# Kernel optimization log

Measured on AMD Instinct MI355X. Metric: run time of the kernel, lower is better.

## Reference

```python
import jax, jax.numpy as jnp
import numpy as np

B, S, D, H, F = 8, 1024, 1024, 16, 4096
DH = D // H  # 64
EPS = 1e-5


def layer_norm(x, g, b):
    mu = jnp.mean(x, axis=-1, keepdims=True)
    var = jnp.mean(jnp.square(x - mu), axis=-1, keepdims=True)
    return (x - mu) * jax.lax.rsqrt(var + EPS) * g + b


def mha(q_in, k_in, v_in, wq, wk, wv, wo, causal):
    # wq/wk/wv: [H, D, DH] (stacked per-head nn.Linear weights, pre-transposed)
    Q = jnp.einsum('bsd,hdk->bhsk', q_in, wq)
    K = jnp.einsum('bsd,hdk->bhsk', k_in, wk)
    V = jnp.einsum('bsd,hdk->bhsk', v_in, wv)
    scores = jnp.einsum('bhsk,bhtk->bhst', Q, K) / jnp.sqrt(jnp.asarray(DH, Q.dtype))
    if causal:
        mask = jnp.triu(jnp.ones((S, S), dtype=bool), k=1)  # True = inaccessible
        scores = jnp.where(mask, -jnp.inf, scores)
    A = jax.nn.softmax(scores, axis=-1)
    heads = jnp.einsum('bhst,bhtk->bhsk', A, V)
    heads = heads.transpose(0, 2, 1, 3).reshape(q_in.shape[0], q_in.shape[1], D)
    return heads @ wo.T  # nn.Linear convention


def setup_inputs() -> dict:
    key = jax.random.key(0)
    ks = jax.random.split(key, 16)
    sc = 1.0 / np.sqrt(D)
    scf = 1.0 / np.sqrt(F)
    return {
        'embeds': jax.random.normal(ks[0], (B, S, D), jnp.float32),
        'encoder_output': jax.random.normal(ks[1], (B, S, D), jnp.float32),
        'wq1': jax.random.normal(ks[2], (H, D, DH), jnp.float32) * sc,
        'wk1': jax.random.normal(ks[3], (H, D, DH), jnp.float32) * sc,
        'wv1': jax.random.normal(ks[4], (H, D, DH), jnp.float32) * sc,
        'wo1': jax.random.normal(ks[5], (D, D), jnp.float32) * sc,
        'wq2': jax.random.normal(ks[6], (H, D, DH), jnp.float32) * sc,
        'wk2': jax.random.normal(ks[7], (H, D, DH), jnp.float32) * sc,
        'wv2': jax.random.normal(ks[8], (H, D, DH), jnp.float32) * sc,
        'wo2': jax.random.normal(ks[9], (D, D), jnp.float32) * sc,
        'ln1_g': jnp.ones((D,), jnp.float32), 'ln1_b': jnp.zeros((D,), jnp.float32),
        'ln2_g': jnp.ones((D,), jnp.float32), 'ln2_b': jnp.zeros((D,), jnp.float32),
        'ln3_g': jnp.ones((D,), jnp.float32), 'ln3_b': jnp.zeros((D,), jnp.float32),
        'w1': jax.random.normal(ks[10], (F, D), jnp.float32) * sc,
        'b1': jnp.zeros((F,), jnp.float32),
        'w2': jax.random.normal(ks[11], (D, F), jnp.float32) * scf,
        'b2': jnp.zeros((D,), jnp.float32),
    }


def reference(embeds, encoder_output, wq1, wk1, wv1, wo1, wq2, wk2, wv2, wo2,
              ln1_g, ln1_b, ln2_g, ln2_b, ln3_g, ln3_b, w1, b1, w2, b2):
    # masked (causal) self-attention + residual + LN
    sa = mha(embeds, embeds, embeds, wq1, wk1, wv1, wo1, causal=True)
    x1 = layer_norm(sa + embeds, ln1_g, ln1_b)
    # cross-attention (no mask) + residual + LN
    ca = mha(x1, encoder_output, encoder_output, wq2, wk2, wv2, wo2, causal=False)
    x2 = layer_norm(ca + x1, ln2_g, ln2_b)
    # feedforward (Linear -> GELU(exact) -> Linear) + residual + LN
    ff = jax.nn.gelu(x2 @ w1.T + b1, approximate=False) @ w2.T + b2
    return layer_norm(ff + x2, ln3_g, ln3_b)
```

## Files before the change

kernel.cpp:

```cpp
#include <hip/hip_runtime.h>
#include <cstdint>
#include <cstddef>

typedef unsigned short u16;
typedef __attribute__((ext_vector_type(4))) float f32x4;
typedef __attribute__((ext_vector_type(4))) float f4;
typedef __attribute__((ext_vector_type(8))) short short8x;
typedef __attribute__((ext_vector_type(4))) u16 u16x4;
typedef __attribute__((ext_vector_type(8))) u16 u16x8;

#define DEV static __device__ __forceinline__

DEV void gl_lds16(const void* g, void* l) {
  __builtin_amdgcn_global_load_lds(
      (const __attribute__((address_space(1))) unsigned int*)g,
      (__attribute__((address_space(3))) unsigned int*)l, 16, 0, 0);
}

DEV u16 f2bf(float f) {
  unsigned u = __float_as_uint(f);
  u += 0x7fffu + ((u >> 16) & 1u);
  return (u16)(u >> 16);
}


__global__ __launch_bounds__(256) void cast_bf16(const float* __restrict__ X, u16* __restrict__ Y) {
  size_t i = ((size_t)blockIdx.x * 256 + threadIdx.x) * 4;
  f4 v = *(const f4*)(X + i);
  u16x4 y;
#pragma unroll
  for (int j = 0; j < 4; ++j) y[j] = f2bf(v[j]);
  *(u16x4*)(Y + i) = y;
}

__global__ __launch_bounds__(256) void cast_wqkv(const float* __restrict__ W, u16* __restrict__ Wt) {
  __shared__ float tile[64][65];
  const int t = threadIdx.x;
  const int h = blockIdx.y;
  const int d0 = blockIdx.x * 64;
  const float* Wb = W + (size_t)h * (1024 * 64);
  const int di = t >> 2;
  const int j0 = (t & 3) * 16;
#pragma unroll
  for (int c = 0; c < 4; ++c) {
    f4 v = *(const f4*)(Wb + (size_t)(d0 + di) * 64 + j0 + c * 4);
#pragma unroll
    for (int j = 0; j < 4; ++j) tile[di][j0 + c * 4 + j] = v[j];
  }
  __syncthreads();
  const int k = t >> 2;
  const int dd0 = (t & 3) * 16;
  u16x8 o0, o1;
#pragma unroll
  for (int u = 0; u < 8; ++u) o0[u] = f2bf(tile[dd0 + u][k]);
#pragma unroll
  for (int u = 0; u < 8; ++u) o1[u] = f2bf(tile[dd0 + 8 + u][k]);
  u16* dst = Wt + (size_t)(h * 64 + k) * 1024 + d0 + dd0;
  *(u16x8*)(dst) = o0;
  *(u16x8*)(dst + 8) = o1;
}

__global__ __launch_bounds__(256) void transpose_v(const u16* __restrict__ V, u16* __restrict__ Vt,
                                                   int vstride, int voff) {
  __shared__ u16 tile[32][72];
  const int t = threadIdx.x;
  const int bh = blockIdx.y;
  const int s0 = blockIdx.x * 32;
  const u16* Vb = V + (size_t)(bh >> 4) * (1024 * (size_t)vstride) + voff + (bh & 15) * 64;
  const int si = t >> 3, d0 = (t & 7) * 8;
  u16x8 val = *(const u16x8*)(Vb + (size_t)(s0 + si) * vstride + d0);
#pragma unroll
  for (int u = 0; u < 8; ++u) tile[si][d0 + u] = val[u];
  __syncthreads();
  const int d = t >> 2, sj0 = (t & 3) * 8;
  u16x8 o;
#pragma unroll
  for (int u = 0; u < 8; ++u) o[u] = tile[sj0 + u][d];
  *(u16x8*)(Vt + (size_t)bh * (64 * 1024) + (size_t)d * 1024 + s0 + sj0) = o;
}

template <int EPI>
__global__ __launch_bounds__(256, 3) void gemm_bt(const u16* __restrict__ A, const u16* __restrict__ Bt,
                                                  void* __restrict__ C, const float* __restrict__ bias,
                                                  int M, int N, int K, int ldc) {
  __shared__ u16 As[2][128 * 32];
  __shared__ u16 Bs[2][128 * 32];
  const int t = threadIdx.x;
  const int wave = t >> 6, lane = t & 63;
  const int lr = lane & 15, lkg = lane >> 4;
  const int swz = (lr >> 1) & 3;
  const int wr = (wave >> 1) * 64, wc = (wave & 1) * 64;
  const int m0 = blockIdx.y * 128, n0 = blockIdx.x * 128;

  const int schunk = ((t & 3) ^ ((t >> 3) & 3)) << 4;
  const char* gA = (const char*)(A + (size_t)(m0 + (t >> 2)) * K) + schunk;
  const char* gB = (const char*)(Bt + (size_t)(n0 + (t >> 2)) * K) + schunk;
  const size_t rowskip = (size_t)64 * K * 2;

  const f32x4 fzero = {0.f, 0.f, 0.f, 0.f};
  f32x4 acc[4][4];
#pragma unroll
  for (int m = 0; m < 4; ++m)
#pragma unroll
    for (int n = 0; n < 4; ++n) acc[m][n] = fzero;

  const int nk = K >> 5;

  auto stage = [&](int buf, int kt) {
    const size_t kb = (size_t)kt * 64;
    char* la = ((char*)&As[buf][0]) + wave * 1024;
    char* lb = ((char*)&Bs[buf][0]) + wave * 1024;
    gl_lds16(gA + kb, la);
    gl_lds16(gA + kb + rowskip, la + 4096);
    gl_lds16(gB + kb, lb);
    gl_lds16(gB + kb + rowskip, lb + 4096);
  };

  auto compute = [&](int buf) {
    const char* as = (const char*)&As[buf][0];
    const char* bs = (const char*)&Bs[buf][0];
    short8x aF[4], bF[4];
#pragma unroll
    for (int m = 0; m < 4; ++m)
      aF[m] = *(const short8x*)(as + (size_t)(wr + m * 16 + lr) * 64 + ((lkg ^ swz) << 4));
#pragma unroll
    for (int n = 0; n < 4; ++n)
      bF[n] = *(const short8x*)(bs + (size_t)(wc + n * 16 + lr) * 64 + ((lkg ^ swz) << 4));
#pragma unroll
    for (int m = 0; m < 4; ++m)
#pragma unroll
      for (int n = 0; n < 4; ++n)
        acc[m][n] = __builtin_amdgcn_mfma_f32_16x16x32_bf16(aF[m], bF[n], acc[m][n], 0, 0, 0);
  };

  stage(0, 0);
  __syncthreads();
  int cur = 0;
  for (int kt = 0; kt < nk; ++kt) {
    if (kt + 1 < nk) stage(cur ^ 1, kt + 1);
    compute(cur);
    __syncthreads();
    cur ^= 1;
  }

#pragma unroll
  for (int m = 0; m < 4; ++m) {
#pragma unroll
    for (int rr = 0; rr < 4; ++rr) {
      const int gm = m0 + wr + m * 16 + lkg * 4 + rr;
#pragma unroll
      for (int n = 0; n < 4; ++n) {
        const int gn = n0 + wc + n * 16 + lr;
        float v = acc[m][n][rr];
        if (EPI == 2 || EPI == 3) v += bias[gn];
        if (EPI == 2) v = 0.5f * v * (1.0f + erff(v * 0.70710678118654752f));
        if (EPI == 4) v *= 0.125f;
        if (EPI == 5 && gn < 1024) v *= 0.125f;
        if (EPI == 1 || EPI == 3)
          ((float*)C)[(size_t)gm * ldc + gn] = v;
        else
          ((u16*)C)[(size_t)gm * ldc + gn] = f2bf(v);
      }
    }
  }
}

template <int CAUSAL>
__global__ __launch_bounds__(256, 2) void flash_attn(const u16* __restrict__ Q, const u16* __restrict__ Kk,
                                                     const u16* __restrict__ Vt, u16* __restrict__ O,
                                                     int qst) {
  __shared__ u16 Ks[2][64 * 64];
  __shared__ u16 Vs[2][64 * 64];
  __shared__ u16 Ps[4][32 * 72];
  const int t = threadIdx.x;
  const int wave = t >> 6, lane = t & 63;
  const int lr = lane & 15, lkg = lane >> 4, lk = lkg * 8;
  const int sw = lr & 7;
  const int bh = blockIdx.y;
  const size_t base = (size_t)(bh >> 4) * (1024 * (size_t)qst) + (bh & 15) * 64;
  const u16* Qb = Q + base;
  const u16* Kb = Kk + base;
  const u16* Vtb = Vt + (size_t)bh * (64 * 1024);
  u16* Ob = O + (size_t)(bh >> 4) * (1024 * 1024) + (bh & 15) * 64;
  const int qt = blockIdx.x * 128;
  const int qw = qt + wave * 32;

  const f32x4 fzero = {0.f, 0.f, 0.f, 0.f};
  short8x qf[2][2];
#pragma unroll
  for (int rb = 0; rb < 2; ++rb)
#pragma unroll
    for (int kk = 0; kk < 2; ++kk)
      qf[rb][kk] = *(const short8x*)(Qb + (size_t)(qw + rb * 16 + lr) * qst + kk * 32 + lk);

  float m_[2][4], l_[2][4];
  f32x4 o_[2][4];
#pragma unroll
  for (int rb = 0; rb < 2; ++rb) {
#pragma unroll
    for (int rr = 0; rr < 4; ++rr) { m_[rb][rr] = -1e30f; l_[rb][rr] = 0.f; }
#pragma unroll
    for (int db = 0; db < 4; ++db) o_[rb][db] = fzero;
  }

  const int rsel = lane >> 3;
  const int csw = ((lane & 7) ^ rsel) << 4;

  auto stage = [&](int buf, int kv0) {
#pragma unroll
    for (int s = 0; s < 2; ++s) {
      const int row = s * 32 + wave * 8 + rsel;
      gl_lds16((const char*)Kb + (size_t)(kv0 + row) * (size_t)(qst * 2) + csw,
               (char*)&Ks[buf][0] + s * 4096 + wave * 1024);
      gl_lds16((const char*)Vtb + (size_t)row * 2048 + (size_t)kv0 * 2 + csw,
               (char*)&Vs[buf][0] + s * 4096 + wave * 1024);
    }
  };

  const int kv_end = CAUSAL ? (qt + 128) : 1024;
  const int nt = kv_end >> 6;

  stage(0, 0);
  __syncthreads();
  int cur = 0;
  for (int tt = 0; tt < nt; ++tt) {
    const int kv0 = tt * 64;
    if (tt + 1 < nt) stage(cur ^ 1, kv0 + 64);

    const char* ksb = (const char*)&Ks[cur][0];
    const char* vsb = (const char*)&Vs[cur][0];

    short8x kf[4][2];
#pragma unroll
    for (int nb = 0; nb < 4; ++nb) {
      const int row = nb * 16 + lr;
#pragma unroll
      for (int kk = 0; kk < 2; ++kk)
        kf[nb][kk] = *(const short8x*)(ksb + row * 128 + (((kk * 4 + lkg) ^ sw) << 4));
    }

#pragma unroll
    for (int rb = 0; rb < 2; ++rb) {
      f32x4 s[4];
#pragma unroll
      for (int nb = 0; nb < 4; ++nb) {
        s[nb] = __builtin_amdgcn_mfma_f32_16x16x32_bf16(qf[rb][0], kf[nb][0], fzero, 0, 0, 0);
        s[nb] = __builtin_amdgcn_mfma_f32_16x16x32_bf16(qf[rb][1], kf[nb][1], s[nb], 0, 0, 0);
      }
      if (CAUSAL && (kv0 + 63 > qw + rb * 16)) {
#pragma unroll
        for (int rr = 0; rr < 4; ++rr) {
          const int qg = qw + rb * 16 + lkg * 4 + rr;
#pragma unroll
          for (int nb = 0; nb < 4; ++nb)
            if (kv0 + nb * 16 + lr > qg) s[nb][rr] = -1e30f;
        }
      }
#pragma unroll
      for (int rr = 0; rr < 4; ++rr) {
        float mx = fmaxf(fmaxf(s[0][rr], s[1][rr]), fmaxf(s[2][rr], s[3][rr]));
#pragma unroll
        for (int d = 1; d < 16; d <<= 1) mx = fmaxf(mx, __shfl_xor(mx, d, 16));
        const float mold = m_[rb][rr];
        const float mnew = fmaxf(mold, mx);
        float p[4];
#pragma unroll
        for (int nb = 0; nb < 4; ++nb) p[nb] = __expf(s[nb][rr] - mnew);
        float rsum = (p[0] + p[1]) + (p[2] + p[3]);
#pragma unroll
        for (int d = 1; d < 16; d <<= 1) rsum += __shfl_xor(rsum, d, 16);
        const float alpha = __expf(mold - mnew);
        m_[rb][rr] = mnew;
        l_[rb][rr] = l_[rb][rr] * alpha + rsum;
#pragma unroll
        for (int db = 0; db < 4; ++db) o_[rb][db][rr] *= alpha;
        const int prow = rb * 16 + lkg * 4 + rr;
#pragma unroll
        for (int nb = 0; nb < 4; ++nb)
          Ps[wave][prow * 72 + nb * 16 + lr] = f2bf(p[nb]);
      }
    }
    asm volatile("s_waitcnt lgkmcnt(0)" ::: "memory");

    short8x vF[4][2];
#pragma unroll
    for (int db = 0; db < 4; ++db) {
      const int row = db * 16 + lr;
#pragma unroll
      for (int kk = 0; kk < 2; ++kk)
        vF[db][kk] = *(const short8x*)(vsb + row * 128 + (((kk * 4 + lkg) ^ sw) << 4));
    }
#pragma unroll
    for (int rb = 0; rb < 2; ++rb) {
#pragma unroll
      for (int kk = 0; kk < 2; ++kk) {
        const short8x aP = *(const short8x*)((const char*)&Ps[wave][0] + (rb * 16 + lr) * 144 + kk * 64 + lkg * 16);
#pragma unroll
        for (int db = 0; db < 4; ++db)
          o_[rb][db] = __builtin_amdgcn_mfma_f32_16x16x32_bf16(aP, vF[db][kk], o_[rb][db], 0, 0, 0);
      }
    }
    __syncthreads();
    cur ^= 1;
  }

#pragma unroll
  for (int rb = 0; rb < 2; ++rb)
#pragma unroll
    for (int rr = 0; rr < 4; ++rr) {
      const float inv = 1.0f / l_[rb][rr];
      const int qg = qw + rb * 16 + lkg * 4 + rr;
#pragma unroll
      for (int db = 0; db < 4; ++db)
        Ob[(size_t)qg * 1024 + db * 16 + lr] = f2bf(o_[rb][db][rr] * inv);
    }
}

__global__ __launch_bounds__(256) void ln_res(const float* __restrict__ X, const float* __restrict__ R,
                                              const float* __restrict__ gam, const float* __restrict__ bet,
                                              float* __restrict__ oF, u16* __restrict__ oB) {
  __shared__ float red[8];
  const int row = blockIdx.x, t = threadIdx.x;
  const int wave = t >> 6, lane = t & 63;
  const size_t off = (size_t)row * 1024 + t * 4;
  f4 x = *(const f4*)(X + off);
  f4 r = *(const f4*)(R + off);
  float v[4];
  float s = 0.f, sq = 0.f;
#pragma unroll
  for (int j = 0; j < 4; ++j) {
    v[j] = x[j] + r[j];
    s += v[j];
    sq += v[j] * v[j];
  }
#pragma unroll
  for (int d = 1; d < 64; d <<= 1) {
    s += __shfl_xor(s, d, 64);
    sq += __shfl_xor(sq, d, 64);
  }
  if (lane == 0) { red[wave * 2] = s; red[wave * 2 + 1] = sq; }
  __syncthreads();
  s = red[0] + red[2] + red[4] + red[6];
  sq = red[1] + red[3] + red[5] + red[7];
  const float mu = s * (1.0f / 1024.0f);
  const float var = sq * (1.0f / 1024.0f) - mu * mu;
  const float rs = rsqrtf(var + 1e-5f);
  f4 g4 = *(const f4*)(gam + t * 4);
  f4 b4 = *(const f4*)(bet + t * 4);
  f4 y;
#pragma unroll
  for (int j = 0; j < 4; ++j) y[j] = (v[j] - mu) * rs * g4[j] + b4[j];
  *(f4*)(oF + off) = y;
  if (oB) {
    u16x4 yb;
#pragma unroll
    for (int j = 0; j < 4; ++j) yb[j] = f2bf(y[j]);
    *(u16x4*)(oB + off) = yb;
  }
}

extern "C" void kernel_launch(void* const* d_in, const int* in_sizes, int n_in,
                              void* d_out, int out_size, void* d_ws, size_t ws_size,
                              hipStream_t stream) {
  const float* embeds = (const float*)d_in[0];
  const float* enc = (const float*)d_in[1];
  const float* wq1 = (const float*)d_in[2];
  const float* wk1 = (const float*)d_in[3];
  const float* wv1 = (const float*)d_in[4];
  const float* wo1 = (const float*)d_in[5];
  const float* wq2 = (const float*)d_in[6];
  const float* wk2 = (const float*)d_in[7];
  const float* wv2 = (const float*)d_in[8];
  const float* wo2 = (const float*)d_in[9];
  const float* ln1g = (const float*)d_in[10];
  const float* ln1b = (const float*)d_in[11];
  const float* ln2g = (const float*)d_in[12];
  const float* ln2b = (const float*)d_in[13];
  const float* ln3g = (const float*)d_in[14];
  const float* ln3b = (const float*)d_in[15];
  const float* w1 = (const float*)d_in[16];
  const float* b1 = (const float*)d_in[17];
  const float* w2 = (const float*)d_in[18];
  const float* b2 = (const float*)d_in[19];
  float* out = (float*)d_out;
  char* ws = (char*)d_ws;
  const size_t MB = (size_t)1 << 20;

  u16* QKV = (u16*)(ws + 0 * MB);
  u16* Vtb = (u16*)(ws + 48 * MB);
  u16* Hd = (u16*)(ws + 64 * MB);
  float* Of = (float*)(ws + 80 * MB);
  u16* ebf = (u16*)(ws + 112 * MB);
  u16* encb = (u16*)(ws + 128 * MB);
  float* x1f = (float*)(ws + 144 * MB);
  float* x2f = (float*)(ws + 176 * MB);
  u16* Wq1t = (u16*)(ws + 208 * MB);
  u16* Wk1t = (u16*)(ws + 210 * MB);
  u16* Wv1t = (u16*)(ws + 212 * MB);
  u16* Wo1b = (u16*)(ws + 214 * MB);
  u16* Wq2t = (u16*)(ws + 216 * MB);
  u16* Wk2t = (u16*)(ws + 218 * MB);
  u16* Wv2t = (u16*)(ws + 220 * MB);
  u16* Wo2b = (u16*)(ws + 222 * MB);
  u16* W1b = (u16*)(ws + 224 * MB);
  u16* W2b = (u16*)(ws + 232 * MB);
  u16* x1b = ebf;
  u16* x2b = encb;
  u16* Hff = (u16*)(ws + 0 * MB);

  dim3 blk(256);

  cast_bf16<<<8192, blk, 0, stream>>>(embeds, ebf);
  cast_bf16<<<8192, blk, 0, stream>>>(enc, encb);
  cast_wqkv<<<dim3(16, 16), blk, 0, stream>>>(wq1, Wq1t);
  cast_wqkv<<<dim3(16, 16), blk, 0, stream>>>(wk1, Wk1t);
  cast_wqkv<<<dim3(16, 16), blk, 0, stream>>>(wv1, Wv1t);
  cast_wqkv<<<dim3(16, 16), blk, 0, stream>>>(wq2, Wq2t);
  cast_wqkv<<<dim3(16, 16), blk, 0, stream>>>(wk2, Wk2t);
  cast_wqkv<<<dim3(16, 16), blk, 0, stream>>>(wv2, Wv2t);
  cast_bf16<<<1024, blk, 0, stream>>>(wo1, Wo1b);
  cast_bf16<<<1024, blk, 0, stream>>>(wo2, Wo2b);
  cast_bf16<<<4096, blk, 0, stream>>>(w1, W1b);
  cast_bf16<<<4096, blk, 0, stream>>>(w2, W2b);

  gemm_bt<5><<<dim3(24, 64), blk, 0, stream>>>(ebf, Wq1t, QKV, nullptr, 8192, 3072, 1024, 3072);
  transpose_v<<<dim3(32, 128), blk, 0, stream>>>(QKV, Vtb, 3072, 2048);
  flash_attn<1><<<dim3(8, 128), blk, 0, stream>>>(QKV, QKV + 1024, Vtb, Hd, 3072);
  gemm_bt<1><<<dim3(8, 64), blk, 0, stream>>>(Hd, Wo1b, Of, nullptr, 8192, 1024, 1024, 1024);
  ln_res<<<8192, blk, 0, stream>>>(Of, embeds, ln1g, ln1b, x1f, x1b);

  gemm_bt<4><<<dim3(8, 64), blk, 0, stream>>>(x1b, Wq2t, QKV, nullptr, 8192, 1024, 1024, 3072);
  gemm_bt<0><<<dim3(16, 64), blk, 0, stream>>>(encb, Wk2t, QKV + 1024, nullptr, 8192, 2048, 1024, 3072);
  transpose_v<<<dim3(32, 128), blk, 0, stream>>>(QKV, Vtb, 3072, 2048);
  flash_attn<0><<<dim3(8, 128), blk, 0, stream>>>(QKV, QKV + 1024, Vtb, Hd, 3072);
  gemm_bt<1><<<dim3(8, 64), blk, 0, stream>>>(Hd, Wo2b, Of, nullptr, 8192, 1024, 1024, 1024);
  ln_res<<<8192, blk, 0, stream>>>(Of, x1f, ln2g, ln2b, x2f, x2b);

  gemm_bt<2><<<dim3(32, 64), blk, 0, stream>>>(x2b, W1b, Hff, b1, 8192, 4096, 1024, 4096);
  gemm_bt<3><<<dim3(8, 64), blk, 0, stream>>>(Hff, W2b, Of, b2, 8192, 1024, 4096, 1024);
  ln_res<<<8192, blk, 0, stream>>>(Of, x2f, ln3g, ln3b, out, nullptr);
}
```

Measured before the change: 762.8 us.

## Replace 128x128 GEMM with 256x256 eight-wave pipelined GEMM

Swaps the 128x128-tile, 4-wave GEMM for a 256x256-tile, 8-wave kernel with K-step 64. It issues split global-to-LDS loads interleaved with MFMA phases, using explicit vmcnt and lgkmcnt waits, barriers and setprio. Workgroup IDs are remapped so consecutive blocks spread across XCDs. The aim is more data reuse per tile and better overlap of loads with matrix math, at the cost of fewer workgroups (e.g. 128 for N=1024 GEMMs), which may leave CUs underused on a 256-CU part.

```diff
diff --git a/kernel.cpp b/kernel.cpp
--- a/kernel.cpp
+++ b/kernel.cpp
@@ -10,6 +10,8 @@
 typedef __attribute__((ext_vector_type(8))) u16 u16x8;
 
 #define DEV static __device__ __forceinline__
+#define VMC(n) asm volatile("s_waitcnt vmcnt(" #n ")" ::: "memory")
+#define LG0() asm volatile("s_waitcnt lgkmcnt(0)" ::: "memory")
 
 DEV void gl_lds16(const void* g, void* l) {
   __builtin_amdgcn_global_load_lds(
@@ -80,77 +82,128 @@
 }
 
 template <int EPI>
-__global__ __launch_bounds__(256, 3) void gemm_bt(const u16* __restrict__ A, const u16* __restrict__ Bt,
+__global__ __launch_bounds__(512, 2) void gemm256(const u16* __restrict__ A, const u16* __restrict__ Bt,
                                                   void* __restrict__ C, const float* __restrict__ bias,
                                                   int M, int N, int K, int ldc) {
-  __shared__ u16 As[2][128 * 32];
-  __shared__ u16 Bs[2][128 * 32];
+  __shared__ u16 lds[65536];
+  char* ldsA = (char*)lds;
+  char* ldsB = (char*)lds + 65536;
   const int t = threadIdx.x;
   const int wave = t >> 6, lane = t & 63;
+  const int wr = wave >> 2, wc = wave & 3;
   const int lr = lane & 15, lkg = lane >> 4;
-  const int swz = (lr >> 1) & 3;
-  const int wr = (wave >> 1) * 64, wc = (wave & 1) * 64;
-  const int m0 = blockIdx.y * 128, n0 = blockIdx.x * 128;
-
-  const int schunk = ((t & 3) ^ ((t >> 3) & 3)) << 4;
-  const char* gA = (const char*)(A + (size_t)(m0 + (t >> 2)) * K) + schunk;
-  const char* gB = (const char*)(Bt + (size_t)(n0 + (t >> 2)) * K) + schunk;
-  const size_t rowskip = (size_t)64 * K * 2;
+  const int swz = lr & 7;
+
+  const int gx = gridDim.x;
+  const int nwg = gx * gridDim.y;
+  const int flat = blockIdx.y * gx + blockIdx.x;
+  const int wg = ((nwg & 7) == 0) ? ((flat & 7) * (nwg >> 3) + (flat >> 3)) : flat;
+  const int m0 = (wg / gx) * 256;
+  const int n0 = (wg % gx) * 256;
+
+  const int nk = K >> 6;
+  const size_t rowb = (size_t)K * 2;
+
+  const int srow = wave * 8 + (lane >> 3);
+  const int sgc = ((lane & 7) ^ (srow & 7)) << 4;
+  const char* gA = (const char*)A + (size_t)(m0 + srow) * rowb + sgc;
+  const char* gB = (const char*)Bt + (size_t)(n0 + srow) * rowb + sgc;
+
+  auto stgA = [&](int kt, int q) {
+    if (kt < nk)
+      gl_lds16(gA + (size_t)(q * 64) * rowb + (size_t)kt * 128,
+               ldsA + ((kt & 1) << 15) + (q << 13) + (wave << 10));
+  };
+  auto stgB = [&](int kt, int q) {
+    if (kt < nk)
+      gl_lds16(gB + (size_t)(q * 64) * rowb + (size_t)kt * 128,
+               ldsB + ((kt & 1) << 15) + (q << 13) + (wave << 10));
+  };
 
   const f32x4 fzero = {0.f, 0.f, 0.f, 0.f};
-  f32x4 acc[4][4];
-#pragma unroll
-  for (int m = 0; m < 4; ++m)
+  f32x4 acc[8][4];
+#pragma unroll
+  for (int m = 0; m < 8; ++m)
 #pragma unroll
     for (int n = 0; n < 4; ++n) acc[m][n] = fzero;
 
-  const int nk = K >> 5;
-
-  auto stage = [&](int buf, int kt) {
-    const size_t kb = (size_t)kt * 64;
-    char* la = ((char*)&As[buf][0]) + wave * 1024;
-    char* lb = ((char*)&Bs[buf][0]) + wave * 1024;
-    gl_lds16(gA + kb, la);
-    gl_lds16(gA + kb + rowskip, la + 4096);
-    gl_lds16(gB + kb, lb);
-    gl_lds16(gB + kb + rowskip, lb + 4096);
-  };
-
-  auto compute = [&](int buf) {
-    const char* as = (const char*)&As[buf][0];
-    const char* bs = (const char*)&Bs[buf][0];
-    short8x aF[4], bF[4];
-#pragma unroll
-    for (int m = 0; m < 4; ++m)
-      aF[m] = *(const short8x*)(as + (size_t)(wr + m * 16 + lr) * 64 + ((lkg ^ swz) << 4));
-#pragma unroll
-    for (int n = 0; n < 4; ++n)
-      bF[n] = *(const short8x*)(bs + (size_t)(wc + n * 16 + lr) * 64 + ((lkg ^ swz) << 4));
-#pragma unroll
-    for (int m = 0; m < 4; ++m)
-#pragma unroll
-      for (int n = 0; n < 4; ++n)
-        acc[m][n] = __builtin_amdgcn_mfma_f32_16x16x32_bf16(aF[m], bF[n], acc[m][n], 0, 0, 0);
-  };
-
-  stage(0, 0);
-  __syncthreads();
-  int cur = 0;
+  stgA(0, 0); stgA(0, 2);
+  stgB(0, 0); stgB(0, 1); stgB(0, 2); stgB(0, 3);
+  stgA(0, 1); stgA(0, 3);
+  stgA(1, 0); stgA(1, 2);
+  VMC(4);
+  __builtin_amdgcn_s_barrier();
+
   for (int kt = 0; kt < nk; ++kt) {
-    if (kt + 1 < nk) stage(cur ^ 1, kt + 1);
-    compute(cur);
-    __syncthreads();
-    cur ^= 1;
-  }
-
-#pragma unroll
-  for (int m = 0; m < 4; ++m) {
+    const char* aB = ldsA + ((kt & 1) << 15);
+    const char* bB = ldsB + ((kt & 1) << 15);
+    short8x aF[4][2], bF[2][2];
+
+    auto rdA = [&](int mh) {
+#pragma unroll
+      for (int mq = 0; mq < 4; ++mq)
+#pragma unroll
+        for (int kh = 0; kh < 2; ++kh)
+          aF[mq][kh] = *(const short8x*)(aB + ((wr * 2 + mh) << 13) + (mq * 16 + lr) * 128 +
+                                         (((kh * 4 + lkg) ^ swz) << 4));
+    };
+    auto rdB = [&](int nh) {
+#pragma unroll
+      for (int nq = 0; nq < 2; ++nq)
+#pragma unroll
+        for (int kh = 0; kh < 2; ++kh)
+          bF[nq][kh] = *(const short8x*)(bB + (wc << 13) + (nh * 32 + nq * 16 + lr) * 128 +
+                                         (((kh * 4 + lkg) ^ swz) << 4));
+    };
+    auto mma = [&](int mh, int nh) {
+      __builtin_amdgcn_s_setprio(1);
+#pragma unroll
+      for (int kh = 0; kh < 2; ++kh)
+#pragma unroll
+        for (int mq = 0; mq < 4; ++mq)
+#pragma unroll
+          for (int nq = 0; nq < 2; ++nq)
+            acc[mh * 4 + mq][nh * 2 + nq] = __builtin_amdgcn_mfma_f32_16x16x32_bf16(
+                aF[mq][kh], bF[nq][kh], acc[mh * 4 + mq][nh * 2 + nq], 0, 0, 0);
+      __builtin_amdgcn_s_setprio(0);
+    };
+
+    rdA(0); rdB(0);
+    stgB(kt + 1, 0); stgB(kt + 1, 1);
+    __builtin_amdgcn_s_barrier();
+    LG0();
+    mma(0, 0);
+    __builtin_amdgcn_s_barrier();
+    rdB(1);
+    stgB(kt + 1, 2); stgB(kt + 1, 3);
+    __builtin_amdgcn_s_barrier();
+    LG0();
+    mma(0, 1);
+    if (kt + 1 < nk) { VMC(6); } else { VMC(0); }
+    __builtin_amdgcn_s_barrier();
+    rdA(1); rdB(0);
+    stgA(kt + 1, 1); stgA(kt + 1, 3);
+    stgA(kt + 2, 0); stgA(kt + 2, 2);
+    __builtin_amdgcn_s_barrier();
+    LG0();
+    mma(1, 0);
+    __builtin_amdgcn_s_barrier();
+    rdB(1);
+    __builtin_amdgcn_s_barrier();
+    LG0();
+    mma(1, 1);
+    if (kt + 2 < nk) { VMC(4); } else if (kt + 1 < nk) { VMC(2); } else { VMC(0); }
+    __builtin_amdgcn_s_barrier();
+  }
+
+#pragma unroll
+  for (int m = 0; m < 8; ++m) {
 #pragma unroll
     for (int rr = 0; rr < 4; ++rr) {
-      const int gm = m0 + wr + m * 16 + lkg * 4 + rr;
+      const int gm = m0 + wr * 128 + m * 16 + lkg * 4 + rr;
 #pragma unroll
       for (int n = 0; n < 4; ++n) {
-        const int gn = n0 + wc + n * 16 + lr;
+        const int gn = n0 + wc * 64 + n * 16 + lr;
         float v = acc[m][n][rr];
         if (EPI == 2 || EPI == 3) v += bias[gn];
         if (EPI == 2) v = 0.5f * v * (1.0f + erff(v * 0.70710678118654752f));
@@ -409,6 +462,7 @@
   u16* Hff = (u16*)(ws + 0 * MB);
 
   dim3 blk(256);
+  dim3 blk512(512);
 
   cast_bf16<<<8192, blk, 0, stream>>>(embeds, ebf);
   cast_bf16<<<8192, blk, 0, stream>>>(enc, encb);
@@ -423,20 +477,20 @@
   cast_bf16<<<4096, blk, 0, stream>>>(w1, W1b);
   cast_bf16<<<4096, blk, 0, stream>>>(w2, W2b);
 
-  gemm_bt<5><<<dim3(24, 64), blk, 0, stream>>>(ebf, Wq1t, QKV, nullptr, 8192, 3072, 1024, 3072);
+  gemm256<5><<<dim3(12, 32), blk512, 0, stream>>>(ebf, Wq1t, QKV, nullptr, 8192, 3072, 1024, 3072);
   transpose_v<<<dim3(32, 128), blk, 0, stream>>>(QKV, Vtb, 3072, 2048);
   flash_attn<1><<<dim3(8, 128), blk, 0, stream>>>(QKV, QKV + 1024, Vtb, Hd, 3072);
-  gemm_bt<1><<<dim3(8, 64), blk, 0, stream>>>(Hd, Wo1b, Of, nullptr, 8192, 1024, 1024, 1024);
+  gemm256<1><<<dim3(4, 32), blk512, 0, stream>>>(Hd, Wo1b, Of, nullptr, 8192, 1024, 1024, 1024);
   ln_res<<<8192, blk, 0, stream>>>(Of, embeds, ln1g, ln1b, x1f, x1b);
 
-  gemm_bt<4><<<dim3(8, 64), blk, 0, stream>>>(x1b, Wq2t, QKV, nullptr, 8192, 1024, 1024, 3072);
-  gemm_bt<0><<<dim3(16, 64), blk, 0, stream>>>(encb, Wk2t, QKV + 1024, nullptr, 8192, 2048, 1024, 3072);
+  gemm256<4><<<dim3(4, 32), blk512, 0, stream>>>(x1b, Wq2t, QKV, nullptr, 8192, 1024, 1024, 3072);
+  gemm256<0><<<dim3(8, 32), blk512, 0, stream>>>(encb, Wk2t, QKV + 1024, nullptr, 8192, 2048, 1024, 3072);
   transpose_v<<<dim3(32, 128), blk, 0, stream>>>(QKV, Vtb, 3072, 2048);
   flash_attn<0><<<dim3(8, 128), blk, 0, stream>>>(QKV, QKV + 1024, Vtb, Hd, 3072);
-  gemm_bt<1><<<dim3(8, 64), blk, 0, stream>>>(Hd, Wo2b, Of, nullptr, 8192, 1024, 1024, 1024);
+  gemm256<1><<<dim3(4, 32), blk512, 0, stream>>>(Hd, Wo2b, Of, nullptr, 8192, 1024, 1024, 1024);
   ln_res<<<8192, blk, 0, stream>>>(Of, x1f, ln2g, ln2b, x2f, x2b);
 
-  gemm_bt<2><<<dim3(32, 64), blk, 0, stream>>>(x2b, W1b, Hff, b1, 8192, 4096, 1024, 4096);
-  gemm_bt<3><<<dim3(8, 64), blk, 0, stream>>>(Hff, W2b, Of, b2, 8192, 1024, 4096, 1024);
+  gemm256<2><<<dim3(16, 32), blk512, 0, stream>>>(x2b, W1b, Hff, b1, 8192, 4096, 1024, 4096);
+  gemm256<3><<<dim3(4, 32), blk512, 0, stream>>>(Hff, W2b, Of, b2, 8192, 1024, 4096, 1024);
   ln_res<<<8192, blk, 0, stream>>>(Of, x2f, ln3g, ln3b, out, nullptr);
 }
```

Measured after the change: 943.5 us. 23.7% more time.

## Replace GEMM with larger 256-row tile, 512-thread kernel with XCD-aware block remap

Applied to the files above, without the earlier changes.

Replaces the 128x128, 256-thread GEMM with a 512-thread kernel using 256xBN tiles and a K-step of 64. It uses an 8-way XOR LDS swizzle, explicit waitcnt, sched_barrier and setprio around the MFMA bursts, and a workgroup index remap that groups blocks by XCD. The aim is more data reuse per LDS load, fewer barriers per K, and better L2 locality on the multi-die GPU. The cost is larger LDS and register use per block (up to 128 KB LDS for BN=256), which lowers occupancy and leaves fewer blocks in the grid for tail balancing.

```diff
diff --git a/kernel.cpp b/kernel.cpp
--- a/kernel.cpp
+++ b/kernel.cpp
@@ -10,6 +10,8 @@
 typedef __attribute__((ext_vector_type(8))) u16 u16x8;
 
 #define DEV static __device__ __forceinline__
+#define VMC0() asm volatile("s_waitcnt vmcnt(0)" ::: "memory")
+#define LG0() asm volatile("s_waitcnt lgkmcnt(0)" ::: "memory")
 
 DEV void gl_lds16(const void* g, void* l) {
   __builtin_amdgcn_global_load_lds(
@@ -79,78 +81,101 @@
   *(u16x8*)(Vt + (size_t)bh * (64 * 1024) + (size_t)d * 1024 + s0 + sj0) = o;
 }
 
-template <int EPI>
-__global__ __launch_bounds__(256, 3) void gemm_bt(const u16* __restrict__ A, const u16* __restrict__ Bt,
+template <int EPI, int BN>
+__global__ __launch_bounds__(512, 2) void gemm2ph(const u16* __restrict__ A, const u16* __restrict__ Bt,
                                                   void* __restrict__ C, const float* __restrict__ bias,
-                                                  int M, int N, int K, int ldc) {
-  __shared__ u16 As[2][128 * 32];
-  __shared__ u16 Bs[2][128 * 32];
+                                                  int K, int ldc) {
+  constexpr int NBQ = BN / 64;
+  constexpr int MR = (BN == 256) ? 8 : 4;
+  __shared__ char ldsA[2][32768];
+  __shared__ char ldsB[2][BN * 128];
+
   const int t = threadIdx.x;
   const int wave = t >> 6, lane = t & 63;
+  const int wr = (BN == 256) ? (wave >> 2) : (wave >> 1);
+  const int wc = (BN == 256) ? (wave & 3) : (wave & 1);
   const int lr = lane & 15, lkg = lane >> 4;
-  const int swz = (lr >> 1) & 3;
-  const int wr = (wave >> 1) * 64, wc = (wave & 1) * 64;
-  const int m0 = blockIdx.y * 128, n0 = blockIdx.x * 128;
-
-  const int schunk = ((t & 3) ^ ((t >> 3) & 3)) << 4;
-  const char* gA = (const char*)(A + (size_t)(m0 + (t >> 2)) * K) + schunk;
-  const char* gB = (const char*)(Bt + (size_t)(n0 + (t >> 2)) * K) + schunk;
-  const size_t rowskip = (size_t)64 * K * 2;
+  const int swz = lr & 7;
+
+  const int gx = gridDim.x;
+  const int nwg = gx * gridDim.y;
+  const int flat = blockIdx.y * gx + blockIdx.x;
+  const int wg = ((nwg & 7) == 0) ? ((flat & 7) * (nwg >> 3) + (flat >> 3)) : flat;
+  const int m0 = (wg / gx) * 256;
+  const int n0 = (wg % gx) * BN;
+
+  const int nk = K >> 6;
+  const size_t rowb = (size_t)K * 2;
+
+  const int srow = wave * 8 + (lane >> 3);
+  const int sgc = ((lane & 7) ^ (srow & 7)) << 4;
+  const char* gA = (const char*)A + (size_t)(m0 + srow) * rowb + sgc;
+  const char* gB = (const char*)Bt + (size_t)(n0 + srow) * rowb + sgc;
+
+  auto stageTile = [&](int buf, int kt) {
+    const size_t kb = (size_t)kt * 128;
+    char* la = &ldsA[buf][0] + (wave << 10);
+    char* lb = &ldsB[buf][0] + (wave << 10);
+#pragma unroll
+    for (int q = 0; q < 4; ++q)
+      gl_lds16(gA + (size_t)(q * 64) * rowb + kb, la + q * 8192);
+#pragma unroll
+    for (int q = 0; q < NBQ; ++q)
+      gl_lds16(gB + (size_t)(q * 64) * rowb + kb, lb + q * 8192);
+  };
 
   const f32x4 fzero = {0.f, 0.f, 0.f, 0.f};
-  f32x4 acc[4][4];
-#pragma unroll
-  for (int m = 0; m < 4; ++m)
+  f32x4 acc[MR][4];
+#pragma unroll
+  for (int m = 0; m < MR; ++m)
 #pragma unroll
     for (int n = 0; n < 4; ++n) acc[m][n] = fzero;
 
-  const int nk = K >> 5;
-
-  auto stage = [&](int buf, int kt) {
-    const size_t kb = (size_t)kt * 64;
-    char* la = ((char*)&As[buf][0]) + wave * 1024;
-    char* lb = ((char*)&Bs[buf][0]) + wave * 1024;
-    gl_lds16(gA + kb, la);
-    gl_lds16(gA + kb + rowskip, la + 4096);
-    gl_lds16(gB + kb, lb);
-    gl_lds16(gB + kb + rowskip, lb + 4096);
-  };
-
-  auto compute = [&](int buf) {
-    const char* as = (const char*)&As[buf][0];
-    const char* bs = (const char*)&Bs[buf][0];
-    short8x aF[4], bF[4];
-#pragma unroll
-    for (int m = 0; m < 4; ++m)
-      aF[m] = *(const short8x*)(as + (size_t)(wr + m * 16 + lr) * 64 + ((lkg ^ swz) << 4));
-#pragma unroll
-    for (int n = 0; n < 4; ++n)
-      bF[n] = *(const short8x*)(bs + (size_t)(wc + n * 16 + lr) * 64 + ((lkg ^ swz) << 4));
-#pragma unroll
-    for (int m = 0; m < 4; ++m)
-#pragma unroll
-      for (int n = 0; n < 4; ++n)
-        acc[m][n] = __builtin_amdgcn_mfma_f32_16x16x32_bf16(aF[m], bF[n], acc[m][n], 0, 0, 0);
-  };
-
-  stage(0, 0);
-  __syncthreads();
+  stageTile(0, 0);
+  VMC0();
+  __builtin_amdgcn_s_barrier();
+
   int cur = 0;
   for (int kt = 0; kt < nk; ++kt) {
-    if (kt + 1 < nk) stage(cur ^ 1, kt + 1);
-    compute(cur);
-    __syncthreads();
+    if (kt + 1 < nk) stageTile(cur ^ 1, kt + 1);
+    const char* aB = &ldsA[cur][0];
+    const char* bB = &ldsB[cur][0];
+#pragma unroll
+    for (int kh = 0; kh < 2; ++kh) {
+      short8x aF[MR], bF[4];
+#pragma unroll
+      for (int m = 0; m < MR; ++m) {
+        const int row = wr * (MR * 16) + m * 16 + lr;
+        aF[m] = *(const short8x*)(aB + row * 128 + (((kh * 4 + lkg) ^ swz) << 4));
+      }
+#pragma unroll
+      for (int n = 0; n < 4; ++n) {
+        const int row = wc * 64 + n * 16 + lr;
+        bF[n] = *(const short8x*)(bB + row * 128 + (((kh * 4 + lkg) ^ swz) << 4));
+      }
+      LG0();
+      __builtin_amdgcn_sched_barrier(0);
+      __builtin_amdgcn_s_setprio(1);
+#pragma unroll
+      for (int m = 0; m < MR; ++m)
+#pragma unroll
+        for (int n = 0; n < 4; ++n)
+          acc[m][n] = __builtin_amdgcn_mfma_f32_16x16x32_bf16(aF[m], bF[n], acc[m][n], 0, 0, 0);
+      __builtin_amdgcn_s_setprio(0);
+    }
+    VMC0();
+    __builtin_amdgcn_s_barrier();
     cur ^= 1;
   }
 
 #pragma unroll
-  for (int m = 0; m < 4; ++m) {
+  for (int m = 0; m < MR; ++m) {
 #pragma unroll
     for (int rr = 0; rr < 4; ++rr) {
-      const int gm = m0 + wr + m * 16 + lkg * 4 + rr;
+      const int gm = m0 + wr * (MR * 16) + m * 16 + lkg * 4 + rr;
 #pragma unroll
       for (int n = 0; n < 4; ++n) {
-        const int gn = n0 + wc + n * 16 + lr;
+        const int gn = n0 + wc * 64 + n * 16 + lr;
         float v = acc[m][n][rr];
         if (EPI == 2 || EPI == 3) v += bias[gn];
         if (EPI == 2) v = 0.5f * v * (1.0f + erff(v * 0.70710678118654752f));
@@ -423,20 +448,20 @@
   cast_bf16<<<4096, blk, 0, stream>>>(w1, W1b);
   cast_bf16<<<4096, blk, 0, stream>>>(w2, W2b);
 
-  gemm_bt<5><<<dim3(24, 64), blk, 0, stream>>>(ebf, Wq1t, QKV, nullptr, 8192, 3072, 1024, 3072);
+  gemm2ph<5, 256><<<dim3(12, 32), 512, 0, stream>>>(ebf, Wq1t, QKV, nullptr, 1024, 3072);
   transpose_v<<<dim3(32, 128), blk, 0, stream>>>(QKV, Vtb, 3072, 2048);
   flash_attn<1><<<dim3(8, 128), blk, 0, stream>>>(QKV, QKV + 1024, Vtb, Hd, 3072);
-  gemm_bt<1><<<dim3(8, 64), blk, 0, stream>>>(Hd, Wo1b, Of, nullptr, 8192, 1024, 1024, 1024);
+  gemm2ph<1, 128><<<dim3(8, 32), 512, 0, stream>>>(Hd, Wo1b, Of, nullptr, 1024, 1024);
   ln_res<<<8192, blk, 0, stream>>>(Of, embeds, ln1g, ln1b, x1f, x1b);
 
-  gemm_bt<4><<<dim3(8, 64), blk, 0, stream>>>(x1b, Wq2t, QKV, nullptr, 8192, 1024, 1024, 3072);
-  gemm_bt<0><<<dim3(16, 64), blk, 0, stream>>>(encb, Wk2t, QKV + 1024, nullptr, 8192, 2048, 1024, 3072);
+  gemm2ph<4, 128><<<dim3(8, 32), 512, 0, stream>>>(x1b, Wq2t, QKV, nullptr, 1024, 3072);
+  gemm2ph<0, 256><<<dim3(8, 32), 512, 0, stream>>>(encb, Wk2t, QKV + 1024, nullptr, 1024, 3072);
   transpose_v<<<dim3(32, 128), blk, 0, stream>>>(QKV, Vtb, 3072, 2048);
   flash_attn<0><<<dim3(8, 128), blk, 0, stream>>>(QKV, QKV + 1024, Vtb, Hd, 3072);
-  gemm_bt<1><<<dim3(8, 64), blk, 0, stream>>>(Hd, Wo2b, Of, nullptr, 8192, 1024, 1024, 1024);
+  gemm2ph<1, 128><<<dim3(8, 32), 512, 0, stream>>>(Hd, Wo2b, Of, nullptr, 1024, 1024);
   ln_res<<<8192, blk, 0, stream>>>(Of, x1f, ln2g, ln2b, x2f, x2b);
 
-  gemm_bt<2><<<dim3(32, 64), blk, 0, stream>>>(x2b, W1b, Hff, b1, 8192, 4096, 1024, 4096);
-  gemm_bt<3><<<dim3(8, 64), blk, 0, stream>>>(Hff, W2b, Of, b2, 8192, 1024, 4096, 1024);
+  gemm2ph<2, 256><<<dim3(16, 32), 512, 0, stream>>>(x2b, W1b, Hff, b1, 1024, 4096);
+  gemm2ph<3, 128><<<dim3(8, 32), 512, 0, stream>>>(Hff, W2b, Of, b2, 4096, 1024);
   ln_res<<<8192, blk, 0, stream>>>(Of, x2f, ln3g, ln3b, out, nullptr);
 }
```

New measurement: 905.9 us. 1.19x slower.

## Add 256x256 eight-wave GEMM with split-K FFN2 and fuse bias into LayerNorm

Applied to the files above, without the earlier changes.

Adds a new 512-thread GEMM kernel with 256x256 tiles, 64-wide K steps, swizzled LDS staging through global_load_lds, a hand-ordered schedule of load and MFMA phases with setprio, and an XCD-aware remapping of workgroup ids. The fused QKV projection, the encoder K/V projection, FFN1 and FFN2 now use this kernel. FFN2 is split-K in two, and the two fp32 partial sums plus the bias b2 are added inside the final LayerNorm. The goal is higher MFMA utilization and more data reuse on the large GEMMs, at the cost of an extra fp32 partial buffer and larger LDS and register use per block.

```diff
diff --git a/kernel.cpp b/kernel.cpp
--- a/kernel.cpp
+++ b/kernel.cpp
@@ -10,6 +10,8 @@
 typedef __attribute__((ext_vector_type(8))) u16 u16x8;
 
 #define DEV static __device__ __forceinline__
+#define VMC(n) asm volatile("s_waitcnt vmcnt(" #n ")" ::: "memory")
+#define LG0() asm volatile("s_waitcnt lgkmcnt(0)" ::: "memory")
 
 DEV void gl_lds16(const void* g, void* l) {
   __builtin_amdgcn_global_load_lds(
@@ -79,10 +81,153 @@
   *(u16x8*)(Vt + (size_t)bh * (64 * 1024) + (size_t)d * 1024 + s0 + sj0) = o;
 }
 
+#define MMA_PHASE(MH, NH, BF)                                                      \
+  {                                                                                \
+    __builtin_amdgcn_s_setprio(1);                                                 \
+    _Pragma("unroll") for (int kh = 0; kh < 2; ++kh)                               \
+        _Pragma("unroll") for (int mq = 0; mq < 4; ++mq)                           \
+            _Pragma("unroll") for (int nq = 0; nq < 2; ++nq)                       \
+                acc[(MH)*4 + mq][(NH)*2 + nq] =                                    \
+                    __builtin_amdgcn_mfma_f32_16x16x32_bf16(                       \
+                        aF[mq][kh], BF[nq][kh], acc[(MH)*4 + mq][(NH)*2 + nq],     \
+                        0, 0, 0);                                                  \
+    __builtin_amdgcn_s_setprio(0);                                                 \
+  }
+
+template <int EPI>
+__global__ __launch_bounds__(512, 2) void gemm8(const u16* __restrict__ A, int lda,
+                                                const u16* __restrict__ Bt, int ldb,
+                                                void* __restrict__ C, int ldc,
+                                                const float* __restrict__ bias,
+                                                int Ksub, long long zCoff) {
+  __shared__ char ldsA[65536];
+  __shared__ char ldsB[65536];
+  const int t = threadIdx.x;
+  const int wave = t >> 6, lane = t & 63;
+  const int wr = wave >> 2, wc = wave & 3;
+  const int lr = lane & 15, lkg = lane >> 4;
+  const int swz = lr & 7;
+
+  const int gx = gridDim.x;
+  const int nwg = gx * gridDim.y;
+  const int flat = blockIdx.y * gx + blockIdx.x;
+  const int wg = (flat & 7) * (nwg >> 3) + (flat >> 3);
+  const int m0 = (wg / gx) * 256;
+  const int n0 = (wg % gx) * 256;
+
+  const int nk = Ksub >> 6;
+  const size_t rowbA = (size_t)lda * 2, rowbB = (size_t)ldb * 2;
+  const size_t kz = (size_t)blockIdx.z * (size_t)Ksub * 2;
+
+  const int srow8 = wave * 8 + (lane >> 3);
+  const int sgc = ((lane & 7) ^ ((lane >> 3) & 7)) << 4;
+  const char* gA = (const char*)A + kz + sgc;
+  const char* gB = (const char*)Bt + kz + sgc;
+
+  auto stgA = [&](int kt, int h) {
+    if (kt >= nk) return;
+    char* dst = ldsA + ((kt & 1) << 15) + (h << 14) + (wave << 10);
+#pragma unroll
+    for (int L = 0; L < 2; ++L)
+      gl_lds16(gA + (size_t)(m0 + h * 64 + L * 128 + srow8) * rowbA + (size_t)kt * 128,
+               dst + L * 8192);
+  };
+  auto stgB = [&](int kt, int h) {
+    if (kt >= nk) return;
+    char* dst = ldsB + ((kt & 1) << 15) + (h << 14) + (wave << 10);
+#pragma unroll
+    for (int L = 0; L < 2; ++L) {
+      const int grow = n0 + (L * 2 + (wave >> 2)) * 64 + h * 32 + (wave & 3) * 8 + (lane >> 3);
+      gl_lds16(gB + (size_t)grow * rowbB + (size_t)kt * 128, dst + L * 8192);
+    }
+  };
+
+  short8x aF[4][2], bF0[2][2], bF1[2][2];
+  auto rdA = [&](int b, int mh) {
+    const char* base = ldsA + (b << 15) + (mh << 14);
+#pragma unroll
+    for (int mq = 0; mq < 4; ++mq)
+#pragma unroll
+      for (int kh = 0; kh < 2; ++kh)
+        aF[mq][kh] = *(const short8x*)(base + (wr * 64 + mq * 16 + lr) * 128 +
+                                       (((kh * 4 + lkg) ^ swz) << 4));
+  };
+  auto rdB = [&](int b, int nh, short8x(&bF)[2][2]) {
+    const char* base = ldsB + (b << 15) + (nh << 14);
+#pragma unroll
+    for (int nq = 0; nq < 2; ++nq)
+#pragma unroll
+      for (int kh = 0; kh < 2; ++kh)
+        bF[nq][kh] = *(const short8x*)(base + (wc * 32 + nq * 16 + lr) * 128 +
+                                       (((kh * 4 + lkg) ^ swz) << 4));
+  };
+
+  const f32x4 fzero = {0.f, 0.f, 0.f, 0.f};
+  f32x4 acc[8][4];
+#pragma unroll
+  for (int m = 0; m < 8; ++m)
+#pragma unroll
+    for (int n = 0; n < 4; ++n) acc[m][n] = fzero;
+
+  stgA(0, 0); stgB(0, 0); stgB(0, 1); stgA(0, 1);
+  VMC(4);
+  stgA(1, 0); stgB(1, 0); stgB(1, 1);
+  VMC(6);
+  __builtin_amdgcn_s_barrier();
+
+  for (int kt = 0; kt < nk; ++kt) {
+    const int b = kt & 1;
+    rdA(b, 0); rdB(b, 0, bF0);
+    stgA(kt + 1, 1);
+    __builtin_amdgcn_s_barrier();
+    LG0(); __builtin_amdgcn_sched_barrier(0);
+    MMA_PHASE(0, 0, bF0);
+    __builtin_amdgcn_s_barrier();
+    rdB(b, 1, bF1);
+    stgA(kt + 2, 0);
+    __builtin_amdgcn_s_barrier();
+    LG0(); __builtin_amdgcn_sched_barrier(0);
+    MMA_PHASE(0, 1, bF1);
+    __builtin_amdgcn_s_barrier();
+    rdA(b, 1);
+    stgB(kt + 2, 0);
+    __builtin_amdgcn_s_barrier();
+    LG0(); __builtin_amdgcn_sched_barrier(0);
+    MMA_PHASE(1, 0, bF0);
+    __builtin_amdgcn_s_barrier();
+    stgB(kt + 2, 1);
+    __builtin_amdgcn_s_barrier();
+    MMA_PHASE(1, 1, bF1);
+    if (kt + 2 < nk) { VMC(6); } else { VMC(0); }
+    __builtin_amdgcn_s_barrier();
+  }
+
+#pragma unroll
+  for (int m = 0; m < 8; ++m) {
+#pragma unroll
+    for (int rr = 0; rr < 4; ++rr) {
+      const int gm = m0 + wr * 128 + (m >> 2) * 64 + (m & 3) * 16 + lkg * 4 + rr;
+#pragma unroll
+      for (int n = 0; n < 4; ++n) {
+        const int gn = n0 + wc * 64 + (n >> 1) * 32 + (n & 1) * 16 + lr;
+        float v = acc[m][n][rr];
+        if (EPI == 2) {
+          v += bias[gn];
+          v = 0.5f * v * (1.0f + erff(v * 0.70710678118654752f));
+        }
+        if (EPI == 5 && gn < 1024) v *= 0.125f;
+        if (EPI == 1)
+          ((float*)C)[(size_t)blockIdx.z * zCoff + (size_t)gm * ldc + gn] = v;
+        else
+          ((u16*)C)[(size_t)gm * ldc + gn] = f2bf(v);
+      }
+    }
+  }
+}
+
 template <int EPI>
 __global__ __launch_bounds__(256, 3) void gemm_bt(const u16* __restrict__ A, const u16* __restrict__ Bt,
-                                                  void* __restrict__ C, const float* __restrict__ bias,
-                                                  int M, int N, int K, int ldc) {
+                                                  void* __restrict__ C, int N, int K, int ldc) {
   __shared__ u16 As[2][128 * 32];
   __shared__ u16 Bs[2][128 * 32];
   const int t = threadIdx.x;
@@ -152,11 +297,8 @@
       for (int n = 0; n < 4; ++n) {
         const int gn = n0 + wc + n * 16 + lr;
         float v = acc[m][n][rr];
-        if (EPI == 2 || EPI == 3) v += bias[gn];
-        if (EPI == 2) v = 0.5f * v * (1.0f + erff(v * 0.70710678118654752f));
         if (EPI == 4) v *= 0.125f;
-        if (EPI == 5 && gn < 1024) v *= 0.125f;
-        if (EPI == 1 || EPI == 3)
+        if (EPI == 1)
           ((float*)C)[(size_t)gm * ldc + gn] = v;
         else
           ((u16*)C)[(size_t)gm * ldc + gn] = f2bf(v);
@@ -316,7 +458,8 @@
     }
 }
 
-__global__ __launch_bounds__(256) void ln_res(const float* __restrict__ X, const float* __restrict__ R,
+__global__ __launch_bounds__(256) void ln_res(const float* __restrict__ X, const float* __restrict__ X2,
+                                              const float* __restrict__ bias, const float* __restrict__ R,
                                               const float* __restrict__ gam, const float* __restrict__ bet,
                                               float* __restrict__ oF, u16* __restrict__ oB) {
   __shared__ float red[8];
@@ -326,13 +469,21 @@
   f4 x = *(const f4*)(X + off);
   f4 r = *(const f4*)(R + off);
   float v[4];
+#pragma unroll
+  for (int j = 0; j < 4; ++j) v[j] = x[j] + r[j];
+  if (X2) {
+    f4 x2 = *(const f4*)(X2 + off);
+#pragma unroll
+    for (int j = 0; j < 4; ++j) v[j] += x2[j];
+  }
+  if (bias) {
+    f4 bb = *(const f4*)(bias + t * 4);
+#pragma unroll
+    for (int j = 0; j < 4; ++j) v[j] += bb[j];
+  }
   float s = 0.f, sq = 0.f;
 #pragma unroll
-  for (int j = 0; j < 4; ++j) {
-    v[j] = x[j] + r[j];
-    s += v[j];
-    sq += v[j] * v[j];
-  }
+  for (int j = 0; j < 4; ++j) { s += v[j]; sq += v[j] * v[j]; }
 #pragma unroll
   for (int d = 1; d < 64; d <<= 1) {
     s += __shfl_xor(s, d, 64);
@@ -423,20 +574,21 @@
   cast_bf16<<<4096, blk, 0, stream>>>(w1, W1b);
   cast_bf16<<<4096, blk, 0, stream>>>(w2, W2b);
 
-  gemm_bt<5><<<dim3(24, 64), blk, 0, stream>>>(ebf, Wq1t, QKV, nullptr, 8192, 3072, 1024, 3072);
+  gemm8<5><<<dim3(12, 32, 1), 512, 0, stream>>>(ebf, 1024, Wq1t, 1024, QKV, 3072, nullptr, 1024, 0);
   transpose_v<<<dim3(32, 128), blk, 0, stream>>>(QKV, Vtb, 3072, 2048);
   flash_attn<1><<<dim3(8, 128), blk, 0, stream>>>(QKV, QKV + 1024, Vtb, Hd, 3072);
-  gemm_bt<1><<<dim3(8, 64), blk, 0, stream>>>(Hd, Wo1b, Of, nullptr, 8192, 1024, 1024, 1024);
-  ln_res<<<8192, blk, 0, stream>>>(Of, embeds, ln1g, ln1b, x1f, x1b);
-
-  gemm_bt<4><<<dim3(8, 64), blk, 0, stream>>>(x1b, Wq2t, QKV, nullptr, 8192, 1024, 1024, 3072);
-  gemm_bt<0><<<dim3(16, 64), blk, 0, stream>>>(encb, Wk2t, QKV + 1024, nullptr, 8192, 2048, 1024, 3072);
+  gemm_bt<1><<<dim3(8, 64), blk, 0, stream>>>(Hd, Wo1b, Of, 1024, 1024, 1024);
+  ln_res<<<8192, blk, 0, stream>>>(Of, nullptr, nullptr, embeds, ln1g, ln1b, x1f, x1b);
+
+  gemm_bt<4><<<dim3(8, 64), blk, 0, stream>>>(x1b, Wq2t, QKV, 1024, 1024, 3072);
+  gemm8<0><<<dim3(8, 32, 1), 512, 0, stream>>>(encb, 1024, Wk2t, 1024, QKV + 1024, 3072, nullptr, 1024, 0);
   transpose_v<<<dim3(32, 128), blk, 0, stream>>>(QKV, Vtb, 3072, 2048);
   flash_attn<0><<<dim3(8, 128), blk, 0, stream>>>(QKV, QKV + 1024, Vtb, Hd, 3072);
-  gemm_bt<1><<<dim3(8, 64), blk, 0, stream>>>(Hd, Wo2b, Of, nullptr, 8192, 1024, 1024, 1024);
-  ln_res<<<8192, blk, 0, stream>>>(Of, x1f, ln2g, ln2b, x2f, x2b);
-
-  gemm_bt<2><<<dim3(32, 64), blk, 0, stream>>>(x2b, W1b, Hff, b1, 8192, 4096, 1024, 4096);
-  gemm_bt<3><<<dim3(8, 64), blk, 0, stream>>>(Hff, W2b, Of, b2, 8192, 1024, 4096, 1024);
-  ln_res<<<8192, blk, 0, stream>>>(Of, x2f, ln3g, ln3b, out, nullptr);
-}
+  gemm_bt<1><<<dim3(8, 64), blk, 0, stream>>>(Hd, Wo2b, Of, 1024, 1024, 1024);
+  ln_res<<<8192, blk, 0, stream>>>(Of, nullptr, nullptr, x1f, ln2g, ln2b, x2f, x2b);
+
+  gemm8<2><<<dim3(16, 32, 1), 512, 0, stream>>>(x2b, 1024, W1b, 1024, Hff, 4096, b1, 1024, 0);
+  gemm8<1><<<dim3(4, 32, 2), 512, 0, stream>>>(Hff, 4096, W2b, 4096, Of, 1024, nullptr, 2048,
+                                               (long long)8192 * 1024);
+  ln_res<<<8192, blk, 0, stream>>>(Of, Of + (size_t)8192 * 1024, b2, x2f, ln3g, ln3b, out, nullptr);
+}
```

New measurement: 872.6 us. +14.4%, slower.
